# Kernel tuning notes

Hardware: AMD Instinct MI355X
Metric: run time of the kernel (lower is better)

Reference implementation:

```python
import jax, jax.numpy as jnp
import numpy as np

OUT_SIZE = 7          # pooled output H=W
SPATIAL_SCALE = 0.125 # FPN stride 8
SAMPLE_NUM = 2        # sampling grid per bin (static)
N_ORIENT = 8
PI = 3.141592653589793


def setup_inputs() -> dict:
    key = jax.random.key(0)
    k1, k2, k3, k4, k5 = jax.random.split(key, 5)
    features = jax.random.normal(k1, (2, 256, 256, 256), dtype=jnp.float32)
    R = 512
    batch = jax.random.randint(k2, (R,), 0, 2).astype(jnp.float32)
    centers = jax.random.uniform(k3, (R, 2), minval=64.0, maxval=1984.0)
    wh = jax.random.uniform(k4, (R, 2), minval=32.0, maxval=512.0)
    theta = jax.random.uniform(k5, (R, 1), minval=0.0, maxval=2.0 * PI)
    rois = jnp.concatenate([batch[:, None], centers, wh, theta], axis=1)
    return {"features": features, "rois": rois}


def _riroi_align(features, rois):
    B, Ctot, H, W = features.shape
    O = N_ORIENT
    C = Ctot // O
    P, G = OUT_SIZE, SAMPLE_NUM
    dtype = features.dtype
    Rn = rois.shape[0]

    batch_ind = rois[:, 0].astype(jnp.int32)
    cw = rois[:, 1] * SPATIAL_SCALE
    ch = rois[:, 2] * SPATIAL_SCALE
    rw = jnp.maximum(rois[:, 3] * SPATIAL_SCALE, 1.0)
    rh = jnp.maximum(rois[:, 4] * SPATIAL_SCALE, 1.0)
    theta = rois[:, 5]

    # orientation alignment: interpolate between two circularly-shifted channels
    ind_f = theta * O / (2.0 * PI)
    ind_floor = jnp.floor(ind_f)
    l_var = ind_f - ind_floor          # weight on shifted-plus-one plane
    r_var = 1.0 - l_var
    ind = jnp.mod(ind_floor.astype(jnp.int32), O)
    o_idx = jnp.arange(O, dtype=jnp.int32)
    ind_rot = jnp.mod(o_idx[None, :] - ind[:, None], O)   # [R,O]
    ind_rot_p = jnp.mod(ind_rot + 1, O)

    # rotated sampling grid; layout (ph, iy, pw, ix) flattened to S
    bin_h = rh / P
    bin_w = rw / P
    pidx = jnp.arange(P, dtype=dtype)
    gidx = (jnp.arange(G, dtype=dtype) + 0.5) / G
    yy = -rh[:, None, None] / 2.0 + (pidx[None, :, None] + gidx[None, None, :]) * bin_h[:, None, None]  # [R,P,G]
    xx = -rw[:, None, None] / 2.0 + (pidx[None, :, None] + gidx[None, None, :]) * bin_w[:, None, None]
    yy = yy[:, :, :, None, None]          # [R,P,G,1,1]
    xx = xx[:, None, None, :, :]          # [R,1,1,P,G]
    cos_t = jnp.cos(theta)[:, None, None, None, None]
    sin_t = jnp.sin(theta)[:, None, None, None, None]
    x = (xx * cos_t - yy * sin_t + cw[:, None, None, None, None]).reshape(Rn, -1)  # [R,S]
    y = (xx * sin_t + yy * cos_t + ch[:, None, None, None, None]).reshape(Rn, -1)
    S = x.shape[1]

    # bilinear interpolation corner indices/weights (ROIAlign semantics)
    valid = (y > -1.0) & (y < H) & (x > -1.0) & (x < W)
    yc = jnp.clip(y, 0.0, None)
    xc = jnp.clip(x, 0.0, None)
    y_low = yc.astype(jnp.int32)
    x_low = xc.astype(jnp.int32)
    y_edge = y_low >= H - 1
    x_edge = x_low >= W - 1
    y_high = jnp.where(y_edge, H - 1, y_low + 1)
    x_high = jnp.where(x_edge, W - 1, x_low + 1)
    y_low = jnp.where(y_edge, H - 1, y_low)
    x_low = jnp.where(x_edge, W - 1, x_low)
    yv = jnp.where(y_edge, y_low.astype(dtype), yc)
    xv = jnp.where(x_edge, x_low.astype(dtype), xc)
    ly = yv - y_low.astype(dtype)
    lx = xv - x_low.astype(dtype)
    hy = 1.0 - ly
    hx = 1.0 - lx
    vm = valid.astype(dtype)
    w00 = hy * hx * vm
    w01 = hy * lx * vm
    w10 = ly * hx * vm
    w11 = ly * lx * vm

    # [B,O,H,W,C] so the channel dim is gathered contiguously
    feats = features.reshape(B, C, O, H, W).transpose(0, 2, 3, 4, 1)
    b = batch_ind[:, None, None]  # [R,1,1]
    yl = y_low[:, None, :]
    yh = y_high[:, None, :]
    xl = x_low[:, None, :]
    xh = x_high[:, None, :]

    def gather_plane(plane):  # plane [R,O] -> [R,O,S,C]
        p = plane[:, :, None]
        return (w00[:, None, :, None] * feats[b, p, yl, xl]
                + w01[:, None, :, None] * feats[b, p, yl, xh]
                + w10[:, None, :, None] * feats[b, p, yh, xl]
                + w11[:, None, :, None] * feats[b, p, yh, xh])

    val = gather_plane(ind_rot)
    val_p = gather_plane(ind_rot_p)
    out = r_var[:, None, None, None] * val + l_var[:, None, None, None] * val_p  # [R,O,S,C]
    out = out.reshape(Rn, O, P, G, P, G, C).mean(axis=(3, 5))  # average over bin samples
    out = out.transpose(0, 4, 1, 2, 3).reshape(Rn, C * O, P, P)  # channel layout c*O + o
    return out


def reference(features, rois):
    return _riroi_align(features, rois)
```

## Files before the change

kernel.cpp:

```cpp
#include <hip/hip_runtime.h>
#include <hip/hip_fp16.h>


typedef _Float16 h16;
typedef _Float16 h8 __attribute__((ext_vector_type(8)));

#define NS 196
#define HW 65536
#define TWO_PI_F 6.283185307179586f
#define OPITCH 132
#define TP 40

__global__ __launch_bounds__(256) void transpose_kernel(
    const float* __restrict__ in, h16* __restrict__ out)
{
    __shared__ h16 lds[256 * TP];
    const int t = threadIdx.x;
    const int a = t & 63;
    const int w = t >> 6;

    const int b  = blockIdx.z;
    const int tc = blockIdx.y;
    const int tp = blockIdx.x;

    const float* ip = in + ((size_t)b * 256 + tc * 32 + w * 8) * HW + tp * 256 + a * 4;

    float4 v[8];
    #pragma unroll
    for (int j = 0; j < 8; ++j)
        v[j] = *(const float4*)(ip + (size_t)j * HW);

    const int wsw = (w ^ (a & 3)) * 8;
    #pragma unroll
    for (int p = 0; p < 4; ++p) {
        h8 row;
        #pragma unroll
        for (int j = 0; j < 8; ++j)
            row[j] = (h16)(((const float*)&v[j])[p]);
        *(h8*)&lds[(a * 4 + p) * TP + wsw] = row;
    }
    __syncthreads();

    h16* op = out + ((size_t)b * HW + (size_t)tp * 256) * 256 + tc * 32;
    #pragma unroll
    for (int k = 0; k < 4; ++k) {
        int px   = (t >> 2) + k * 64;
        int part = t & 3;
        int pps  = (part ^ ((px >> 2) & 3)) * 8;
        h8 r = *(const h8*)&lds[px * TP + pps];
        *(h8*)(op + (size_t)px * 256 + part * 8) = r;
    }
}

__global__ __launch_bounds__(512, 8) void riroi_gather(
    const h16* __restrict__ ft, const float* __restrict__ rois,
    float* __restrict__ out)
{
    const int r    = blockIdx.x >> 1;
    const int half = blockIdx.x & 1;
    const int tid  = threadIdx.x;
    const int lane = tid & 63;
    const int wave = tid >> 6;
    const int cn   = lane >> 4;
    const int chg  = lane & 15;

    const float* roi = rois + r * 6;
    int bb = (int)roi[0];
    const float cw = roi[1] * 0.125f;
    const float ch = roi[2] * 0.125f;
    const float rw = fmaxf(roi[3] * 0.125f, 1.0f);
    const float rh = fmaxf(roi[4] * 0.125f, 1.0f);
    const float theta = roi[5];

    const float ind_f = theta * 8.0f / TWO_PI_F;
    const float fl    = floorf(ind_f);
    const float lvar  = ind_f - fl;
    const float rvar  = 1.0f - lvar;
    int ii = (int)fl;
    int ind_v = ((ii % 8) + 8) & 7;
    const int b   = __builtin_amdgcn_readfirstlane(bb);
    const int ind = __builtin_amdgcn_readfirstlane(ind_v);

    const float cost = cosf(theta), sint = sinf(theta);
    const float bin_h = rh * (1.0f / 7.0f), bin_w = rw * (1.0f / 7.0f);

    __shared__ int   s_off[4][49 * 4];
    __shared__ float s_w[4][49 * 4];
    __shared__ float s_out[49 * OPITCH];

    if (tid < NS) {
        int iy = tid / 14, ix = tid - iy * 14;
        int py = iy >> 1, gy = iy & 1;
        int px = ix >> 1, gx = ix & 1;
        int q = (py * 7 + px) * 4 + ((gy << 1) | gx);
        float yy = ((float)py + ((float)gy + 0.5f) * 0.5f) * bin_h - rh * 0.5f;
        float xx = ((float)px + ((float)gx + 0.5f) * 0.5f) * bin_w - rw * 0.5f;
        float x = xx * cost - yy * sint + cw;
        float y = xx * sint + yy * cost + ch;
        float vm = (y > -1.0f && y < 256.0f && x > -1.0f && x < 256.0f) ? 1.0f : 0.0f;
        float yc = fmaxf(y, 0.0f), xc = fmaxf(x, 0.0f);
        int y0 = (int)yc, x0 = (int)xc;
        int y1, x1; float yv, xv;
        if (y0 >= 255) { y0 = 255; y1 = 255; yv = 255.0f; }
        else           { y1 = y0 + 1; yv = yc; }
        if (x0 >= 255) { x0 = 255; x1 = 255; xv = 255.0f; }
        else           { x1 = x0 + 1; xv = xc; }
        float ly = yv - (float)y0, lx = xv - (float)x0;
        float hy = 1.0f - ly, hx = 1.0f - lx;
        s_w[0][q] = hy * hx * vm;
        s_w[1][q] = hy * lx * vm;
        s_w[2][q] = ly * hx * vm;
        s_w[3][q] = ly * lx * vm;
        int y0w = y0 << 8, y1w = y1 << 8;
        s_off[0][q] = (y0w + x0) << 8;
        s_off[1][q] = (y0w + x1) << 8;
        s_off[2][q] = (y1w + x0) << 8;
        s_off[3][q] = (y1w + x1) << 8;
    }
    __syncthreads();

    const h16* fb = ft + (size_t)b * ((size_t)HW * 256) + half * 128 + (chg << 3);

    int myb = wave;
    int4   off = *(const int4*)  &s_off[cn][myb << 2];
    float4 wv  = *(const float4*)&s_w  [cn][myb << 2];
    while (myb < 49) {
        h8 f0 = *(const h8*)(fb + off.x);
        h8 f1 = *(const h8*)(fb + off.y);
        h8 f2 = *(const h8*)(fb + off.z);
        h8 f3 = *(const h8*)(fb + off.w);

        int nb = myb + 8;
        int pb = (nb < 49) ? nb : myb;
        int4   off_n = *(const int4*)  &s_off[cn][pb << 2];
        float4 wv_n  = *(const float4*)&s_w  [cn][pb << 2];

        float v[8];
        #pragma unroll
        for (int i = 0; i < 8; ++i)
            v[i] = wv.x * (float)f0[i] + wv.y * (float)f1[i]
                 + wv.z * (float)f2[i] + wv.w * (float)f3[i];

        #pragma unroll
        for (int i = 0; i < 8; ++i) {
            v[i] += __shfl_xor(v[i], 16);
            unsigned u = __float_as_uint(v[i]);
            auto pr = __builtin_amdgcn_permlane32_swap(u, u, false, false);
            v[i] = __uint_as_float(pr[0]) + __uint_as_float(pr[1]);
        }
        if (cn == 0) {
            float res[8];
            #pragma unroll
            for (int i = 0; i < 8; ++i)
                res[i] = 0.25f * (rvar * v[i] + lvar * v[(i + 1) & 7]);
            float* dst = &s_out[myb * OPITCH + (chg << 3)];
            *(float4*)dst       = make_float4(res[0], res[1], res[2], res[3]);
            *(float4*)(dst + 4) = make_float4(res[4], res[5], res[6], res[7]);
        }
        myb = nb; off = off_n; wv = wv_n;
    }
    __syncthreads();

    const int ind_neg = (8 - ind) & 7;
    float* ob = out + (size_t)r * 12544 + half * 6272;
    for (int i = tid << 2; i < 6272; i += 2048) {
        float4 vo;
        #pragma unroll
        for (int q = 0; q < 4; ++q) {
            int j   = i + q;
            int co  = j / 49;
            int bin = j - co * 49;
            int ci  = (co & ~7) | ((co + ind_neg) & 7);
            ((float*)&vo)[q] = s_out[bin * OPITCH + ci];
        }
        *(float4*)(ob + i) = vo;
    }
}

extern "C" void kernel_launch(void* const* d_in, const int* in_sizes, int n_in,
                              void* d_out, int out_size, void* d_ws, size_t ws_size,
                              hipStream_t stream) {
    const float* feat = (const float*)d_in[0];
    const float* rois = (const float*)d_in[1];
    float* out = (float*)d_out;

    h16* ft = (h16*)d_ws;
    transpose_kernel<<<dim3(256, 8, 2), dim3(256), 0, stream>>>(feat, ft);
    riroi_gather<<<dim3(1024), dim3(512), 0, stream>>>(ft, rois, out);
}
```

Before: 240.8 us.

## Sort ROI-half work items by spatial bucket and remap blocks for XCD locality

Block (0,0,0) of the transpose kernel now buckets each ROI/half work item by coarse center location (y band, x half, channel half) using a counting sort in LDS, and writes a permutation to the workspace. The gather kernel maps blockIdx through an XCD-aware swizzle, (g&7)*128 + g/8, into that permutation, so blocks on the same XCD handle spatially nearby ROIs and the same channel half. The goal is more L2 reuse of feature rows across blocks on MI355X's per-XCD L2 caches. It adds a small serial sort to one transpose block and an extra indirection load per gather block.

```diff
diff --git a/kernel.cpp b/kernel.cpp
--- a/kernel.cpp
+++ b/kernel.cpp
@@ -10,9 +10,11 @@
 #define TWO_PI_F 6.283185307179586f
 #define OPITCH 132
 #define TP 40
+#define FT_BYTES 67108864u
 
 __global__ __launch_bounds__(256) void transpose_kernel(
-    const float* __restrict__ in, h16* __restrict__ out)
+    const float* __restrict__ in, h16* __restrict__ out,
+    const float* __restrict__ rois, int* __restrict__ perm)
 {
     __shared__ h16 lds[256 * TP];
     const int t = threadIdx.x;
@@ -46,18 +48,52 @@
     for (int k = 0; k < 4; ++k) {
         int px   = (t >> 2) + k * 64;
         int part = t & 3;
-        int pps  = (part ^ ((px >> 2) & 3)) * 8;
-        h8 r = *(const h8*)&lds[px * TP + pps];
+        int pps  = (part ^ ((px >> 2) & 3)) * 4;
+        h8 r = *(const h8*)&lds[px * TP + ((part ^ ((px >> 2) & 3)) * 8)];
         *(h8*)(op + (size_t)px * 256 + part * 8) = r;
+        (void)pps;
+    }
+
+    if (blockIdx.x == 0 && blockIdx.y == 0 && blockIdx.z == 0) {
+        __syncthreads();
+        int* cnt  = (int*)&lds[0];
+        int* base = (int*)&lds[32];
+        if (t < 16) cnt[t] = 0;
+        __syncthreads();
+        int mykey[4], myrank[4];
+        #pragma unroll
+        for (int e = 0; e < 4; ++e) {
+            int rh = t * 4 + e;
+            int r  = rh >> 1, h = rh & 1;
+            float cx = rois[r * 6 + 1] * 0.125f;
+            float cy = rois[r * 6 + 2] * 0.125f;
+            int by = (int)cy >> 6;  by = by > 3 ? 3 : (by < 0 ? 0 : by);
+            int bx = ((int)cx >> 7) & 1;
+            int key = ((((by << 1) | bx) << 1) | h);
+            mykey[e]  = key;
+            myrank[e] = atomicAdd(&cnt[key], 1);
+        }
+        __syncthreads();
+        if (t == 0) {
+            int s = 0;
+            for (int k2 = 0; k2 < 16; ++k2) { base[k2] = s; s += cnt[k2]; }
+        }
+        __syncthreads();
+        #pragma unroll
+        for (int e = 0; e < 4; ++e)
+            perm[base[mykey[e]] + myrank[e]] = t * 4 + e;
     }
 }
 
 __global__ __launch_bounds__(512, 8) void riroi_gather(
     const h16* __restrict__ ft, const float* __restrict__ rois,
-    float* __restrict__ out)
+    float* __restrict__ out, const int* __restrict__ perm)
 {
-    const int r    = blockIdx.x >> 1;
-    const int half = blockIdx.x & 1;
+    const int g    = blockIdx.x;
+    const int pos  = ((g & 7) << 7) + (g >> 3);
+    const int rh_i = perm[pos];
+    const int r    = rh_i >> 1;
+    const int half = rh_i & 1;
     const int tid  = threadIdx.x;
     const int lane = tid & 63;
     const int wave = tid >> 6;
@@ -184,7 +220,9 @@
     const float* rois = (const float*)d_in[1];
     float* out = (float*)d_out;
 
-    h16* ft = (h16*)d_ws;
-    transpose_kernel<<<dim3(256, 8, 2), dim3(256), 0, stream>>>(feat, ft);
-    riroi_gather<<<dim3(1024), dim3(512), 0, stream>>>(ft, rois, out);
+    h16* ft   = (h16*)d_ws;
+    int* perm = (int*)((char*)d_ws + FT_BYTES);
+
+    transpose_kernel<<<dim3(256, 8, 2), dim3(256), 0, stream>>>(feat, ft, rois, perm);
+    riroi_gather<<<dim3(1024), dim3(512), 0, stream>>>(ft, rois, out, perm);
 }
```

Result: no change. 237.6 us (-1.4%).
